# Optimization experiments

Hardware: AMD Instinct MI355X
Metric: run time of the kernel (lower is better)

Reference implementation:

```python
import jax, jax.numpy as jnp
import numpy as np
from jax import lax

N = 8192
TARGET_COMPONENTS = 1.0
TARGET_CYCLES = 0.0
WEIGHT = 1.0
THRESH_SHIFT = 2.0


def setup_inputs() -> dict:
    key = jax.random.key(0)
    x = jax.random.normal(key, (N, N), dtype=jnp.float32)
    # symmetrize so directed DFS traversal == undirected connectivity,
    # then shift so adj > 0 is sparse (realistic learned graph structure)
    adj = (x + x.T) * 0.5 - THRESH_SHIFT
    return {"adj": adj}


def _count_components(adj):
    """Connected components via min-label propagation (parallel equivalent
    of the serial DFS in the torch module for a symmetric adjacency)."""
    n = adj.shape[0]
    pos = adj > 0  # [n, n] bool edge mask
    labels0 = jnp.arange(n, dtype=jnp.int32)

    def body(state):
        labels, _ = state
        # min label among neighbors (n = sentinel for non-edges)
        neigh_min = jnp.min(jnp.where(pos, labels[None, :], jnp.int32(n)), axis=1)
        new_labels = jnp.minimum(labels, neigh_min)
        return new_labels, jnp.any(new_labels != labels)

    labels, _ = lax.while_loop(lambda s: s[1], body,
                               (labels0, jnp.array(True)))
    # exactly one node per component keeps its own (minimal) index
    return jnp.sum((labels == labels0).astype(jnp.int32))


def reference(adj):
    n = adj.shape[0]
    n_comp = _count_components(adj).astype(jnp.float32)
    n_edges = (jnp.sum((adj > 0).astype(jnp.int32)) // 2).astype(jnp.float32)
    betti_1 = n_edges - jnp.float32(n) + n_comp           # Betti-1 estimate
    n_cycles = jnp.maximum(jnp.float32(0.0), betti_1)
    component_loss = (n_comp - TARGET_COMPONENTS) ** 2
    cycle_loss = (n_cycles - TARGET_CYCLES) ** 2
    return WEIGHT * (component_loss + cycle_loss)
```

## Files before the change

kernel.cpp:

```cpp
#include <hip/hip_runtime.h>


#define NN 8192
#define SCAN_LDS_CAP 2048

__global__ __launch_bounds__(64) void init_kernel(int* counters) {
    if (threadIdx.x < 2) counters[threadIdx.x] = 0;
}

__global__ __launch_bounds__(256) void scan_kernel(const float* __restrict__ adj,
                                                   int* __restrict__ counters,
                                                   unsigned int* __restrict__ ebuf,
                                                   int cap) {
    __shared__ int lds_n;
    __shared__ int lds_base;
    __shared__ unsigned int lds_e[SCAN_LDS_CAP];
    if (threadIdx.x == 0) lds_n = 0;
    __syncthreads();

    int b = blockIdx.x;
    int c1 = 0;

    #pragma unroll
    for (int half = 0; half < 2; ++half) {
        int r = half ? (NN - 1 - b) : b;
        const float4* rowp = (const float4*)(adj + (size_t)r * NN);
        int nf4 = (r + 4) >> 2;

        auto process = [&](float4 v, int g) {
            int j0 = g << 2;
            float vv[4] = {v.x, v.y, v.z, v.w};
            #pragma unroll
            for (int c = 0; c < 4; ++c) {
                int j = j0 + c;
                bool pos = vv[c] > 0.0f;
                if (pos && j < r) {
                    int k = atomicAdd(&lds_n, 1);
                    unsigned int e = ((unsigned)r << 13) | (unsigned)j;
                    if (k < SCAN_LDS_CAP) lds_e[k] = e;
                    else {
                        int gk = atomicAdd(counters, 1);
                        if (gk < cap) ebuf[gk] = e;
                    }
                }
                c1 += (pos && j == r) ? 1 : 0;
            }
        };

        int g = threadIdx.x;
        for (; g + 768 < nf4; g += 1024) {
            float4 v0 = rowp[g];
            float4 v1 = rowp[g + 256];
            float4 v2 = rowp[g + 512];
            float4 v3 = rowp[g + 768];
            process(v0, g);
            process(v1, g + 256);
            process(v2, g + 512);
            process(v3, g + 768);
        }
        for (; g < nf4; g += 256) process(rowp[g], g);
    }

    #pragma unroll
    for (int off = 32; off > 0; off >>= 1) c1 += __shfl_down(c1, off, 64);
    if ((threadIdx.x & 63) == 0 && c1) atomicAdd(counters + 1, c1);

    __syncthreads();
    int n = lds_n < SCAN_LDS_CAP ? lds_n : SCAN_LDS_CAP;
    if (threadIdx.x == 0) lds_base = atomicAdd(counters, n);
    __syncthreads();
    int base = lds_base;
    for (int k = threadIdx.x; k < n; k += 256) {
        int idx = base + k;
        if (idx < cap) ebuf[idx] = lds_e[k];
    }
}

__global__ __launch_bounds__(1024) void label_final_kernel(
        const unsigned int* __restrict__ ebuf,
        const int* __restrict__ counters,
        int cap, float* __restrict__ out) {
    __shared__ int lab[NN];
    __shared__ int changed;
    __shared__ int wsum[16];
    int tid = threadIdx.x;
    for (int i = tid; i < NN; i += 1024) lab[i] = i;
    __syncthreads();

    int total_lower = counters[0];
    int m = total_lower < cap ? total_lower : cap;

    for (;;) {
        if (tid == 0) changed = 0;
        __syncthreads();

        for (int i = tid; i < m; i += 1024) {
            unsigned int e = ebuf[i];
            int r = (int)(e >> 13);
            int j = (int)(e & (NN - 1));
            int lr = lab[r];
            int lj = lab[j];
            if (lj < lr) {
                int old = atomicMin(&lab[r], lj);
                if (lj < old) changed = 1;
            } else if (lr < lj) {
                int old = atomicMin(&lab[j], lr);
                if (lr < old) changed = 1;
            }
        }
        __syncthreads();

        for (int i = tid; i < NN; i += 1024) {
            int l = lab[i];
            int ll = lab[l];
            if (ll < l) { lab[i] = ll; changed = 1; }
        }
        __syncthreads();

        if (changed == 0) break;
        __syncthreads();
    }

    int cnt = 0;
    for (int i = tid; i < NN; i += 1024) cnt += (lab[i] == i) ? 1 : 0;
    #pragma unroll
    for (int off = 32; off > 0; off >>= 1) cnt += __shfl_down(cnt, off, 64);
    if ((tid & 63) == 0) wsum[tid >> 6] = cnt;
    __syncthreads();
    if (tid == 0) {
        int roots = 0;
        #pragma unroll
        for (int w = 0; w < 16; ++w) roots += wsum[w];
        long long total = 2LL * (long long)total_lower + (long long)counters[1];
        long long n_edges_i = total >> 1;
        double n_comp = (double)roots;
        double comp_loss = (n_comp - 1.0) * (n_comp - 1.0);
        double betti = (double)n_edges_i - (double)NN + n_comp;
        double cyc = betti > 0.0 ? betti : 0.0;
        out[0] = (float)(comp_loss + cyc * cyc);
    }
}

extern "C" void kernel_launch(void* const* d_in, const int* in_sizes, int n_in,
                              void* d_out, int out_size, void* d_ws, size_t ws_size,
                              hipStream_t stream) {
    const float* adj = (const float*)d_in[0];
    int* ws = (int*)d_ws;
    int* counters = ws;
    unsigned int* ebuf = (unsigned int*)(ws + 2);
    long long cap_ll = (long long)(ws_size / 4) - 2;
    int cap = cap_ll > 0x7fffffff ? 0x7fffffff : (cap_ll < 0 ? 0 : (int)cap_ll);
    float* out = (float*)d_out;

    init_kernel<<<1, 64, 0, stream>>>(counters);
    scan_kernel<<<NN / 2, 256, 0, stream>>>(adj, counters, ebuf, cap);
    label_final_kernel<<<1, 1024, 0, stream>>>(ebuf, counters, cap, out);
}
```

Before: 414.5 us.

## Use per-block edge segments, prefix-sum compaction, and hooking union-find with edge filtering

The scan kernel now runs 2048 blocks of four rows each and writes edges to fixed per-block segments with per-block counts, so the global atomic counters and the init kernel are no longer needed. The single-block label kernel prefix-sums the counts and compacts the segments into one edge array. It then runs hooking-style union-find (atomicMin on both the node and its root), followed by pointer jumping to convergence. After each round it drops edges whose endpoints already share a label, so later rounds touch fewer edges. A final verification loop checks convergence. The costs are a serial per-thread compaction copy done in a single block and fixed workspace assumptions (segment cap SEG, ACAP) that rely on a large workspace.

```diff
diff --git a/kernel.cpp b/kernel.cpp
--- a/kernel.cpp
+++ b/kernel.cpp
@@ -2,28 +2,29 @@
 
 
 #define NN 8192
-#define SCAN_LDS_CAP 2048
-
-__global__ __launch_bounds__(64) void init_kernel(int* counters) {
-    if (threadIdx.x < 2) counters[threadIdx.x] = 0;
-}
+#define NBLK 2048
+#define SEG 2048
+#define ACAP (1 << 22)
 
 __global__ __launch_bounds__(256) void scan_kernel(const float* __restrict__ adj,
-                                                   int* __restrict__ counters,
-                                                   unsigned int* __restrict__ ebuf,
-                                                   int cap) {
+                                                   unsigned int* __restrict__ ws) {
     __shared__ int lds_n;
-    __shared__ int lds_base;
-    __shared__ unsigned int lds_e[SCAN_LDS_CAP];
+    __shared__ unsigned int lds_e[SEG];
+    __shared__ int wsum[4];
     if (threadIdx.x == 0) lds_n = 0;
     __syncthreads();
 
+    unsigned int* cnt = ws;
+    unsigned int* dcnt = ws + NBLK;
+    unsigned int* seg = ws + 2 * NBLK + (size_t)blockIdx.x * SEG;
+
     int b = blockIdx.x;
+    int rows[4] = { b, NN - 1 - b, NN / 2 - 1 - b, NN / 2 + b };
     int c1 = 0;
 
     #pragma unroll
-    for (int half = 0; half < 2; ++half) {
-        int r = half ? (NN - 1 - b) : b;
+    for (int t = 0; t < 4; ++t) {
+        int r = rows[t];
         const float4* rowp = (const float4*)(adj + (size_t)r * NN);
         int nf4 = (r + 4) >> 2;
 
@@ -36,12 +37,7 @@
                 bool pos = vv[c] > 0.0f;
                 if (pos && j < r) {
                     int k = atomicAdd(&lds_n, 1);
-                    unsigned int e = ((unsigned)r << 13) | (unsigned)j;
-                    if (k < SCAN_LDS_CAP) lds_e[k] = e;
-                    else {
-                        int gk = atomicAdd(counters, 1);
-                        if (gk < cap) ebuf[gk] = e;
-                    }
+                    if (k < SEG) lds_e[k] = ((unsigned)r << 13) | (unsigned)j;
                 }
                 c1 += (pos && j == r) ? 1 : 0;
             }
@@ -53,85 +49,146 @@
             float4 v1 = rowp[g + 256];
             float4 v2 = rowp[g + 512];
             float4 v3 = rowp[g + 768];
-            process(v0, g);
-            process(v1, g + 256);
-            process(v2, g + 512);
-            process(v3, g + 768);
+            process(v0, g); process(v1, g + 256);
+            process(v2, g + 512); process(v3, g + 768);
         }
         for (; g < nf4; g += 256) process(rowp[g], g);
     }
 
     #pragma unroll
     for (int off = 32; off > 0; off >>= 1) c1 += __shfl_down(c1, off, 64);
-    if ((threadIdx.x & 63) == 0 && c1) atomicAdd(counters + 1, c1);
-
-    __syncthreads();
-    int n = lds_n < SCAN_LDS_CAP ? lds_n : SCAN_LDS_CAP;
-    if (threadIdx.x == 0) lds_base = atomicAdd(counters, n);
-    __syncthreads();
-    int base = lds_base;
-    for (int k = threadIdx.x; k < n; k += 256) {
-        int idx = base + k;
-        if (idx < cap) ebuf[idx] = lds_e[k];
-    }
+    if ((threadIdx.x & 63) == 0) wsum[threadIdx.x >> 6] = c1;
+    __syncthreads();
+
+    int n = lds_n < SEG ? lds_n : SEG;
+    if (threadIdx.x == 0) {
+        cnt[b] = (unsigned)n;
+        dcnt[b] = (unsigned)(wsum[0] + wsum[1] + wsum[2] + wsum[3]);
+    }
+    for (int k = threadIdx.x; k < n; k += 256) seg[k] = lds_e[k];
 }
 
 __global__ __launch_bounds__(1024) void label_final_kernel(
-        const unsigned int* __restrict__ ebuf,
-        const int* __restrict__ counters,
-        int cap, float* __restrict__ out) {
+        unsigned int* __restrict__ ws, float* __restrict__ out) {
     __shared__ int lab[NN];
-    __shared__ int changed;
+    __shared__ int sA[NBLK], sB[NBLK];
+    __shared__ int nact, fch, vch;
     __shared__ int wsum[16];
     int tid = threadIdx.x;
+
+    unsigned int* cnt = ws;
+    unsigned int* dcnt = ws + NBLK;
+    unsigned int* segs = ws + 2 * NBLK;
+    unsigned int* A = segs + (size_t)NBLK * SEG;
+    unsigned int* B = A + ACAP;
+    unsigned int* C = B + ACAP;
+
     for (int i = tid; i < NN; i += 1024) lab[i] = i;
-    __syncthreads();
-
-    int total_lower = counters[0];
-    int m = total_lower < cap ? total_lower : cap;
+
+    int diag_local = 0;
+    for (int i = tid; i < NBLK; i += 1024) {
+        sA[i] = (int)cnt[i];
+        diag_local += (int)dcnt[i];
+    }
+    __syncthreads();
+    int* src = sA; int* dst = sB;
+    for (int d = 1; d < NBLK; d <<= 1) {
+        for (int i = tid; i < NBLK; i += 1024)
+            dst[i] = src[i] + (i >= d ? src[i - d] : 0);
+        __syncthreads();
+        int* t2 = src; src = dst; dst = t2;
+    }
+    int total_lower = src[NBLK - 1];
+
+    for (int bb = tid; bb < NBLK; bb += 1024) {
+        int n = (int)cnt[bb];
+        int base = src[bb] - n;
+        const unsigned int* s = segs + (size_t)bb * SEG;
+        for (int k = 0; k < n; ++k) A[base + k] = s[k];
+    }
+    __syncthreads();
+
+    int m = total_lower;
+    unsigned int* cur = A;
+    unsigned int* nxt = B;
+
+    while (m > 0) {
+        for (int i = tid; i < m; i += 1024) {
+            unsigned int e = cur[i];
+            int r = (int)(e >> 13), j = (int)(e & (NN - 1));
+            int lr = lab[r], lj = lab[j];
+            if (lj < lr)      { atomicMin(&lab[r], lj); atomicMin(&lab[lr], lj); }
+            else if (lr < lj) { atomicMin(&lab[j], lr); atomicMin(&lab[lj], lr); }
+        }
+        __syncthreads();
+        for (;;) {
+            if (tid == 0) fch = 0;
+            __syncthreads();
+            for (int i = tid; i < NN; i += 1024) {
+                int l = lab[i]; int ll = lab[l];
+                if (ll < l) { lab[i] = ll; fch = 1; }
+            }
+            __syncthreads();
+            if (fch == 0) break;
+            __syncthreads();
+        }
+        if (tid == 0) nact = 0;
+        __syncthreads();
+        for (int i = tid; i < m; i += 1024) {
+            unsigned int e = cur[i];
+            int a = lab[e >> 13], b2 = lab[e & (NN - 1)];
+            if (a != b2) {
+                int hi = a > b2 ? a : b2, lo = a ^ b2 ^ hi;
+                nxt[atomicAdd(&nact, 1)] = ((unsigned)hi << 13) | (unsigned)lo;
+            }
+        }
+        __syncthreads();
+        m = nact;
+        cur = nxt;
+        nxt = (cur == B) ? C : B;
+    }
 
     for (;;) {
-        if (tid == 0) changed = 0;
-        __syncthreads();
-
-        for (int i = tid; i < m; i += 1024) {
-            unsigned int e = ebuf[i];
-            int r = (int)(e >> 13);
-            int j = (int)(e & (NN - 1));
-            int lr = lab[r];
-            int lj = lab[j];
-            if (lj < lr) {
-                int old = atomicMin(&lab[r], lj);
-                if (lj < old) changed = 1;
-            } else if (lr < lj) {
-                int old = atomicMin(&lab[j], lr);
-                if (lr < old) changed = 1;
-            }
-        }
-        __syncthreads();
-
-        for (int i = tid; i < NN; i += 1024) {
-            int l = lab[i];
-            int ll = lab[l];
-            if (ll < l) { lab[i] = ll; changed = 1; }
-        }
-        __syncthreads();
-
-        if (changed == 0) break;
-        __syncthreads();
-    }
-
-    int cnt = 0;
-    for (int i = tid; i < NN; i += 1024) cnt += (lab[i] == i) ? 1 : 0;
-    #pragma unroll
-    for (int off = 32; off > 0; off >>= 1) cnt += __shfl_down(cnt, off, 64);
-    if ((tid & 63) == 0) wsum[tid >> 6] = cnt;
+        for (;;) {
+            if (tid == 0) fch = 0;
+            __syncthreads();
+            for (int i = tid; i < NN; i += 1024) {
+                int l = lab[i]; int ll = lab[l];
+                if (ll < l) { lab[i] = ll; fch = 1; }
+            }
+            __syncthreads();
+            if (fch == 0) break;
+            __syncthreads();
+        }
+        if (tid == 0) vch = 0;
+        __syncthreads();
+        for (int i = tid; i < total_lower; i += 1024) {
+            unsigned int e = A[i];
+            int r = (int)(e >> 13), j = (int)(e & (NN - 1));
+            int lr = lab[r], lj = lab[j];
+            if (lj < lr)      { atomicMin(&lab[r], lj); vch = 1; }
+            else if (lr < lj) { atomicMin(&lab[j], lr); vch = 1; }
+        }
+        __syncthreads();
+        if (vch == 0) break;
+        __syncthreads();
+    }
+
+    int cnt_roots = 0;
+    for (int i = tid; i < NN; i += 1024) cnt_roots += (lab[i] == i) ? 1 : 0;
+    #pragma unroll
+    for (int off = 32; off > 0; off >>= 1)
+        cnt_roots += __shfl_down(cnt_roots, off, 64);
+    #pragma unroll
+    for (int off = 32; off > 0; off >>= 1)
+        diag_local += __shfl_down(diag_local, off, 64);
+    if ((tid & 63) == 0) { wsum[tid >> 6] = cnt_roots; sA[tid >> 6] = diag_local; }
     __syncthreads();
     if (tid == 0) {
-        int roots = 0;
+        int roots = 0, diag = 0;
         #pragma unroll
-        for (int w = 0; w < 16; ++w) roots += wsum[w];
-        long long total = 2LL * (long long)total_lower + (long long)counters[1];
+        for (int w = 0; w < 16; ++w) { roots += wsum[w]; diag += sA[w]; }
+        long long total = 2LL * (long long)total_lower + (long long)diag;
         long long n_edges_i = total >> 1;
         double n_comp = (double)roots;
         double comp_loss = (n_comp - 1.0) * (n_comp - 1.0);
@@ -145,14 +202,9 @@
                               void* d_out, int out_size, void* d_ws, size_t ws_size,
                               hipStream_t stream) {
     const float* adj = (const float*)d_in[0];
-    int* ws = (int*)d_ws;
-    int* counters = ws;
-    unsigned int* ebuf = (unsigned int*)(ws + 2);
-    long long cap_ll = (long long)(ws_size / 4) - 2;
-    int cap = cap_ll > 0x7fffffff ? 0x7fffffff : (cap_ll < 0 ? 0 : (int)cap_ll);
+    unsigned int* ws = (unsigned int*)d_ws;
     float* out = (float*)d_out;
 
-    init_kernel<<<1, 64, 0, stream>>>(counters);
-    scan_kernel<<<NN / 2, 256, 0, stream>>>(adj, counters, ebuf, cap);
-    label_final_kernel<<<1, 1024, 0, stream>>>(ebuf, counters, cap, out);
+    scan_kernel<<<NBLK, 256, 0, stream>>>(adj, ws);
+    label_final_kernel<<<1, 1024, 0, stream>>>(ws, out);
 }
```

Measured after the change: 537.1 us. 1.3x slower.
